# Optimization experiments

Hardware: AMD Instinct MI355X
Metric: run time of the kernel (lower is better)

Reference implementation:

```python
import jax, jax.numpy as jnp
import numpy as np
import math

N = 50000      # nodes per view
E = 800000     # edges per view (avg degree 16)
V = 2          # number of views / adjacencies
F_IN = 500     # input feature dim per view
C = 128        # nhidden
L = 4          # nlayers
NCLASS = 16
K_ATT = 5      # ECA kernel: t=int((log2(128)+1)/2)=4 -> even -> k=5
ALPHA = 0.1
LAMDA = 0.5


def setup_inputs() -> dict:
    key = jax.random.key(0)
    ks = jax.random.split(key, 12)
    glorot = lambda k, shp: jax.random.uniform(k, shp, jnp.float32, -1.0, 1.0) * np.sqrt(6.0 / (shp[-1] + shp[-2]))
    return {
        'x': jax.random.normal(ks[0], (V, N, F_IN), jnp.float32),
        'rows': jax.random.randint(ks[1], (V, E), 0, N, jnp.int32),
        'cols': jax.random.randint(ks[2], (V, E), 0, N, jnp.int32),
        # normalized-adjacency-like values, ~1/deg so spmm output stays O(1)
        'vals': jax.random.uniform(ks[3], (V, E), jnp.float32) / 16.0,
        'fc_w': glorot(ks[4], (V, C, F_IN)),
        'fc_b': jnp.zeros((V, C), jnp.float32),
        'conv_w': glorot(ks[5], (L, C, C)),
        'att_conv_w': jax.random.normal(ks[6], (L, K_ATT), jnp.float32) * (1.0 / np.sqrt(K_ATT)),
        'att_fc_w': glorot(ks[7], (L, C, C)),
        'att_fc_b': jnp.zeros((L, C), jnp.float32),
        'att_mix_w': jnp.full((L,), -0.8, jnp.float32),
        'out_w': glorot(ks[8], (NCLASS, C)),
        'out_b': jnp.zeros((NCLASS,), jnp.float32),
    }


def _conv1d(x, w):
    # torch Conv1d(1,1,k,padding=k//2,bias=False) over channel axis; x:[N,C], w:[k]
    k = w.shape[0]
    pad = k // 2
    xp = jnp.pad(x, ((0, 0), (pad, pad)))
    c = x.shape[1]
    out = jnp.zeros_like(x)
    for j in range(k):  # k is small & static (5)
        out = out + w[j] * xp[:, j:j + c]
    return out


def _fc_attention(xv, cw, fw, fb, mw):
    # xv:[N,C]. AdaptiveAvgPool2d(1) on a [N,C,1,1] tensor is identity.
    x1 = _conv1d(xv, cw)                 # [N,C]
    x2 = xv @ fw.T + fb                  # 1x1 conv2d == linear, [N,C]
    # sum over dim=1 of the [N,C,C] outer products == (row-sum) * other vector
    s1 = jnp.sum(x1, axis=1, keepdims=True)
    s2 = jnp.sum(x2, axis=1, keepdims=True)
    out1 = jax.nn.sigmoid(s1 * x2)
    out2 = jax.nn.sigmoid(s2 * x1)
    m = jax.nn.sigmoid(mw)
    out = m * out1 + (1.0 - m) * out2
    out = jax.nn.sigmoid(_conv1d(out, cw))
    return xv * out, out


def _ortho_norm(W):
    wtw = W.T @ W + 1e-4 * jnp.eye(W.shape[1], dtype=W.dtype)
    Lc = jnp.linalg.cholesky(wtw)
    # W @ inv(Lc).T  ==  solve_triangular(Lc, W.T).T
    return jax.scipy.linalg.solve_triangular(Lc, W.T, lower=True).T


def _gcn_layer(h, r, c, v, h0, W, l):
    Wo = _ortho_norm(W)
    hi = jax.ops.segment_sum(v[:, None] * h[c], r, num_segments=h.shape[0])  # spmm
    support = (1.0 - ALPHA) * hi + ALPHA * h0
    theta = math.log(LAMDA / l + 1.0)
    out = theta * (support @ Wo) + (1.0 - theta) * support  # residual=False, variant=False
    return jnp.tanh(out)


def reference(x, rows, cols, vals, fc_w, fc_b, conv_w, att_conv_w, att_fc_w,
              att_fc_b, att_mix_w, out_w, out_b):
    weights_att = []
    outputs = []
    for k in range(V):
        h0 = jax.nn.relu(x[k] @ fc_w[k].T + fc_b[k])  # dropout is identity in eval
        h = h0
        for i in range(L):
            if k == 0:
                h, w_att = _fc_attention(h, att_conv_w[i], att_fc_w[i], att_fc_b[i], att_mix_w[i])
                weights_att.append(w_att)
                h = jax.nn.relu(_gcn_layer(h, rows[k], cols[k], vals[k], h0, conv_w[i], i + 1))
            else:
                h = jax.nn.relu(_gcn_layer(h, rows[k], cols[k], vals[k], h0, conv_w[i], i + 1))
                h = h * weights_att[i]
        outputs.append(h)
    logits = [o @ out_w.T + out_b for o in outputs]
    total = logits[0]
    for lg in logits[1:]:
        total = total + lg
    lsm = [jax.nn.log_softmax(lg, axis=1) for lg in logits]
    mean_out = jnp.mean(jnp.stack(lsm), axis=0)
    return (jax.nn.log_softmax(total, axis=1), mean_out, lsm[0], lsm[1])
```

## Files before the change

### kernel.cpp

```cpp
#include <hip/hip_runtime.h>
#include <hip/hip_bf16.h>
#include <math.h>

static const int N_NODES = 50000;
static const int N_EDGES = 800000;
static const int F_IN    = 500;
static const int C_DIM   = 128;

using bf16x8 = __attribute__((ext_vector_type(8))) short;
using f32x4  = __attribute__((ext_vector_type(4))) float;

__device__ __forceinline__ float sigmoidf_(float x) { return 1.f / (1.f + __expf(-x)); }

__device__ __forceinline__ unsigned short f2bf(float f) {
    __hip_bfloat16 h = __float2bfloat16(f);
    unsigned short u;
    __builtin_memcpy(&u, &h, 2);
    return u;
}

__global__ __launch_bounds__(256) void wtw_kernel(const float* __restrict__ conv_w,
                                                  float* __restrict__ Am_g)
{
    __shared__ float Wi[128][16];
    __shared__ float Wj[128][16];
    const int bid = blockIdx.x;
    const int li  = bid >> 6;
    const int t6  = bid & 63;
    const int ti  = (t6 >> 3) << 4;
    const int tj  = (t6 & 7) << 4;
    const int tid = threadIdx.x;
    const float* W = conv_w + (size_t)li * 16384;
    for (int idx = tid; idx < 2048; idx += 256) {
        int k = idx >> 4, c = idx & 15;
        Wi[k][c] = W[k * 128 + ti + c];
        Wj[k][c] = W[k * 128 + tj + c];
    }
    __syncthreads();
    const int i = tid >> 4, j = tid & 15;
    float acc = 0.f;
    for (int k = 0; k < 128; ++k) acc = fmaf(Wi[k][i], Wj[k][j], acc);
    if (ti + i == tj + j) acc += 1e-4f;
    Am_g[(size_t)li * 16384 + (ti + i) * 128 + tj + j] = acc;
}

__global__ __launch_bounds__(512) void chol_solve_kernel(const float* __restrict__ Am_g,
                                                         const float* __restrict__ conv_w,
                                                         unsigned short* __restrict__ woT)
{
    __shared__ float Am[128][129];
    __shared__ float Wm[128][129];
    const int li  = blockIdx.x;
    const int tid = threadIdx.x;
    const float* Ag = Am_g  + (size_t)li * 16384;
    const float* Wg = conv_w + (size_t)li * 16384;
    for (int idx = tid; idx < 16384; idx += 512) {
        Am[idx >> 7][idx & 127] = Ag[idx];
        Wm[idx >> 7][idx & 127] = Wg[idx];
    }
    __syncthreads();

    for (int k = 0; k < 127; ++k) {
        float rk = 1.f / Am[k][k];
        const int R = 127 - k;
        for (int idx = tid; idx < (R << 7); idx += 512) {
            int i2 = k + 1 + (idx >> 7);
            int j  = idx & 127;
            if (j > k && j <= i2)
                Am[i2][j] = fmaf(-Am[i2][k] * rk, Am[j][k], Am[i2][j]);
        }
        __syncthreads();
    }

    for (int p = 0; p < 4; ++p) {
        const int kbase = p * 32;
        if (p > 0) {
            const int kk = tid & 31, k = kbase + kk;
            const int jb = (tid >> 5) * 8;
            float a0=0,a1=0,a2=0,a3=0,a4=0,a5=0,a6=0,a7=0;
            for (int m = 0; m < kbase; ++m) {
                float am = Am[k][m];
                a0 = fmaf(am, Wm[jb+0][m], a0); a1 = fmaf(am, Wm[jb+1][m], a1);
                a2 = fmaf(am, Wm[jb+2][m], a2); a3 = fmaf(am, Wm[jb+3][m], a3);
                a4 = fmaf(am, Wm[jb+4][m], a4); a5 = fmaf(am, Wm[jb+5][m], a5);
                a6 = fmaf(am, Wm[jb+6][m], a6); a7 = fmaf(am, Wm[jb+7][m], a7);
            }
            Wm[jb+0][k] -= a0; Wm[jb+1][k] -= a1; Wm[jb+2][k] -= a2; Wm[jb+3][k] -= a3;
            Wm[jb+4][k] -= a4; Wm[jb+5][k] -= a5; Wm[jb+6][k] -= a6; Wm[jb+7][k] -= a7;
        }
        __syncthreads();
        if (tid < 128) {
            const int j = tid;
            for (int kk = 0; kk < 32; ++kk) {
                int k = kbase + kk;
                float num = Wm[j][k];
                for (int m = kbase; m < k; ++m) num = fmaf(-Am[k][m], Wm[j][m], num);
                Wm[j][k] = num / Am[k][k];
            }
        }
        __syncthreads();
    }

    unsigned short* o = woT + (size_t)li * 16384;
    for (int idx = tid; idx < 16384; idx += 512) {
        int a = idx >> 7, b = idx & 127;
        o[idx] = f2bf(Wm[b][a] * sqrtf(Am[a][a]));
    }
}

__global__ __launch_bounds__(256) void conv_attw_kernel(const float* __restrict__ w,
                                                        unsigned short* __restrict__ o)
{
    int idx = blockIdx.x * 256 + threadIdx.x;
    if (idx < 65536) o[idx] = f2bf(w[idx]);
}

__global__ __launch_bounds__(256) void conv_fcw_kernel(const float* __restrict__ w,
                                                       unsigned short* __restrict__ o)
{
    int idx = blockIdx.x * 256 + threadIdx.x;
    if (idx >= 131072) return;
    int row = idx >> 9, k = idx & 511;
    o[idx] = (k < 500) ? f2bf(w[row * 500 + k]) : (unsigned short)0;
}


__global__ __launch_bounds__(256) void fc_relu_mfma_kernel(const float* __restrict__ x,
                                                           const unsigned short* __restrict__ wbf,
                                                           const float* __restrict__ b,
                                                           float* __restrict__ h0,
                                                           float* __restrict__ h1,
                                                           int nrows)
{
    __shared__ unsigned short Asm[64 * 136];
    __shared__ unsigned short Bsm[128 * 136];
    const int tid  = threadIdx.x;
    const int n0   = blockIdx.x * 64;
    const int lane = tid & 63;
    const int wv   = tid >> 6;
    const int lrow = lane & 15;
    const int kgrp = lane >> 4;

    f32x4 acc[8];
#pragma unroll
    for (int t = 0; t < 8; ++t) acc[t] = (f32x4){0.f, 0.f, 0.f, 0.f};

    for (int kc = 0; kc < 512; kc += 128) {
        for (int cid = tid; cid < 128 * 16; cid += 256) {
            int r = cid >> 4, c8 = cid & 15;
            *reinterpret_cast<bf16x8*>(&Bsm[r * 136 + c8 * 8]) =
                *reinterpret_cast<const bf16x8*>(&wbf[r * 512 + kc + c8 * 8]);
        }
        for (int cid = tid; cid < 64 * 16; cid += 256) {
            int r = cid >> 4, c8 = cid & 15;
            int n = n0 + r;
            int kg = kc + c8 * 8;
            union { unsigned short u[8]; bf16x8 v; } t;
            if (n < nrows && kg + 8 <= 500) {
                const float* src = &x[(size_t)n * 500 + kg];
                float4 v0 = *reinterpret_cast<const float4*>(src);
                float4 v1 = *reinterpret_cast<const float4*>(src + 4);
                t.u[0]=f2bf(v0.x); t.u[1]=f2bf(v0.y); t.u[2]=f2bf(v0.z); t.u[3]=f2bf(v0.w);
                t.u[4]=f2bf(v1.x); t.u[5]=f2bf(v1.y); t.u[6]=f2bf(v1.z); t.u[7]=f2bf(v1.w);
            } else if (n < nrows) {
#pragma unroll
                for (int e = 0; e < 8; ++e)
                    t.u[e] = (kg + e < 500) ? f2bf(x[(size_t)n * 500 + kg + e]) : (unsigned short)0;
            } else {
#pragma unroll
                for (int e = 0; e < 8; ++e) t.u[e] = 0;
            }
            *reinterpret_cast<bf16x8*>(&Asm[r * 136 + c8 * 8]) = t.v;
        }
        __syncthreads();
#pragma unroll
        for (int kt = 0; kt < 4; ++kt) {
            int koff = kt * 32 + kgrp * 8;
            bf16x8 av = *reinterpret_cast<const bf16x8*>(&Asm[(wv * 16 + lrow) * 136 + koff]);
#pragma unroll
            for (int t = 0; t < 8; ++t) {
                bf16x8 bv = *reinterpret_cast<const bf16x8*>(&Bsm[(t * 16 + lrow) * 136 + koff]);
                acc[t] = __builtin_amdgcn_mfma_f32_16x16x32_bf16(av, bv, acc[t], 0, 0, 0);
            }
        }
        __syncthreads();
    }
#pragma unroll
    for (int t = 0; t < 8; ++t) {
        int j = t * 16 + lrow;
        float bj = b[j];
#pragma unroll
        for (int r = 0; r < 4; ++r) {
            int n = n0 + wv * 16 + kgrp * 4 + r;
            if (n < nrows) {
                float v = fmaxf(acc[t][r] + bj, 0.f);
                h0[(size_t)n * 128 + j] = v;
                h1[(size_t)n * 128 + j] = v;
            }
        }
    }
}

template <int MODE>
__global__ __launch_bounds__(256) void gemm128_mfma_kernel(const float* __restrict__ A0,
                                                           const float* __restrict__ A1,
                                                           const unsigned short* __restrict__ Bw,
                                                           const float* __restrict__ bias,
                                                           const float* __restrict__ watt,
                                                           float* __restrict__ outp,
                                                           float c0, float c1, float theta,
                                                           int nrows)
{
    __shared__ unsigned short Asm[64 * 136];
    __shared__ unsigned short Bsm[128 * 136];
    const int tid  = threadIdx.x;
    const int n0   = blockIdx.x * 64;
    const int lane = tid & 63;
    const int wv   = tid >> 6;
    const int lrow = lane & 15;
    const int kgrp = lane >> 4;

    for (int cid = tid; cid < 128 * 16; cid += 256) {
        int r = cid >> 4, c8 = cid & 15;
        *reinterpret_cast<bf16x8*>(&Bsm[r * 136 + c8 * 8]) =
            *reinterpret_cast<const bf16x8*>(&Bw[r * 128 + c8 * 8]);
    }
    for (int cid = tid; cid < 64 * 16; cid += 256) {
        int r = cid >> 4, c8 = cid & 15;
        int n = n0 + r;
        union { unsigned short u[8]; bf16x8 v; } t;
        if (n < nrows) {
            const float* s0 = &A0[(size_t)n * 128 + c8 * 8];
            float4 a0 = *reinterpret_cast<const float4*>(s0);
            float4 a1 = *reinterpret_cast<const float4*>(s0 + 4);
            if (MODE == 1) {
                const float* s1 = &A1[(size_t)n * 128 + c8 * 8];
                float4 b0 = *reinterpret_cast<const float4*>(s1);
                float4 b1 = *reinterpret_cast<const float4*>(s1 + 4);
                a0.x = c0 * a0.x + c1 * b0.x; a0.y = c0 * a0.y + c1 * b0.y;
                a0.z = c0 * a0.z + c1 * b0.z; a0.w = c0 * a0.w + c1 * b0.w;
                a1.x = c0 * a1.x + c1 * b1.x; a1.y = c0 * a1.y + c1 * b1.y;
                a1.z = c0 * a1.z + c1 * b1.z; a1.w = c0 * a1.w + c1 * b1.w;
            }
            t.u[0]=f2bf(a0.x); t.u[1]=f2bf(a0.y); t.u[2]=f2bf(a0.z); t.u[3]=f2bf(a0.w);
            t.u[4]=f2bf(a1.x); t.u[5]=f2bf(a1.y); t.u[6]=f2bf(a1.z); t.u[7]=f2bf(a1.w);
        } else {
#pragma unroll
            for (int e = 0; e < 8; ++e) t.u[e] = 0;
        }
        *reinterpret_cast<bf16x8*>(&Asm[r * 136 + c8 * 8]) = t.v;
    }
    __syncthreads();

    f32x4 acc[8];
#pragma unroll
    for (int t = 0; t < 8; ++t) acc[t] = (f32x4){0.f, 0.f, 0.f, 0.f};
#pragma unroll
    for (int kt = 0; kt < 4; ++kt) {
        int koff = kt * 32 + kgrp * 8;
        bf16x8 av = *reinterpret_cast<const bf16x8*>(&Asm[(wv * 16 + lrow) * 136 + koff]);
#pragma unroll
        for (int t = 0; t < 8; ++t) {
            bf16x8 bv = *reinterpret_cast<const bf16x8*>(&Bsm[(t * 16 + lrow) * 136 + koff]);
            acc[t] = __builtin_amdgcn_mfma_f32_16x16x32_bf16(av, bv, acc[t], 0, 0, 0);
        }
    }

#pragma unroll
    for (int t = 0; t < 8; ++t) {
        int j = t * 16 + lrow;
#pragma unroll
        for (int r = 0; r < 4; ++r) {
            int n = n0 + wv * 16 + kgrp * 4 + r;
            if (n >= nrows) continue;
            float v = acc[t][r];
            if (MODE == 0) {
                v += bias[j];
            } else {
                float s = c0 * A0[(size_t)n * 128 + j] + c1 * A1[(size_t)n * 128 + j];
                v = theta * v + (1.f - theta) * s;
                v = tanhf(v);
                v = fmaxf(v, 0.f);
                if (watt) v *= watt[(size_t)n * 128 + j];
            }
            outp[(size_t)n * 128 + j] = v;
        }
    }
}

__global__ __launch_bounds__(256) void att_kernel(float* __restrict__ h,
                                                  const float* __restrict__ x2g,
                                                  const float* __restrict__ cw,
                                                  const float* __restrict__ mwp,
                                                  float* __restrict__ watt,
                                                  int nrows)
{
    __shared__ float hrow[2][132];
    __shared__ float orow[2][132];
    __shared__ float red[2][2][2];
    const int tid = threadIdx.x;
    const int c   = tid & 127;
    const int rl  = tid >> 7;
    const int n   = blockIdx.x * 2 + rl;
    const bool valid = n < nrows;
    float hv = 0.f, x2v = 0.f;
    if (valid) { hv = h[(size_t)n * 128 + c]; x2v = x2g[(size_t)n * 128 + c]; }
    hrow[rl][c + 2] = hv;
    if (c < 2) { hrow[rl][c] = 0.f; hrow[rl][c + 130] = 0.f; }
    const float w0 = cw[0], w1 = cw[1], w2 = cw[2], w3 = cw[3], w4 = cw[4];
    __syncthreads();
    float x1 = w0 * hrow[rl][c] + w1 * hrow[rl][c + 1] + w2 * hrow[rl][c + 2]
             + w3 * hrow[rl][c + 3] + w4 * hrow[rl][c + 4];
    float p1 = x1, p2 = x2v;
#pragma unroll
    for (int off = 32; off; off >>= 1) { p1 += __shfl_xor(p1, off); p2 += __shfl_xor(p2, off); }
    int wir = (tid >> 6) & 1;
    if ((tid & 63) == 0) { red[rl][0][wir] = p1; red[rl][1][wir] = p2; }
    __syncthreads();
    float s1 = red[rl][0][0] + red[rl][0][1];
    float s2 = red[rl][1][0] + red[rl][1][1];
    float m  = sigmoidf_(mwp[0]);
    float o  = m * sigmoidf_(s1 * x2v) + (1.f - m) * sigmoidf_(s2 * x1);
    orow[rl][c + 2] = o;
    if (c < 2) { orow[rl][c] = 0.f; orow[rl][c + 130] = 0.f; }
    __syncthreads();
    float wv = w0 * orow[rl][c] + w1 * orow[rl][c + 1] + w2 * orow[rl][c + 2]
             + w3 * orow[rl][c + 3] + w4 * orow[rl][c + 4];
    wv = sigmoidf_(wv);
    if (valid) {
        watt[(size_t)n * 128 + c] = wv;
        h[(size_t)n * 128 + c]    = hv * wv;
    }
}

__global__ __launch_bounds__(256) void hist_kernel(const int* __restrict__ rows,
                                                   int* __restrict__ rcnt)
{
    int gid = blockIdx.x * 256 + threadIdx.x;
    if (gid >= 2 * N_EDGES) return;
    int vsel = (gid >= N_EDGES) ? 1 : 0;
    atomicAdd(&rcnt[vsel * N_NODES + rows[gid]], 1);
}

__global__ __launch_bounds__(1024) void scan_kernel(int* __restrict__ rcnt)
{
    __shared__ int s[2][1024];
    int* c = rcnt + blockIdx.x * N_NODES;
    const int tid = threadIdx.x;
    int running = 0;
    for (int base = 0; base < N_NODES; base += 1024) {
        int idx = base + tid;
        int val = (idx < N_NODES) ? c[idx] : 0;
        int buf = 0;
        s[0][tid] = val;
        __syncthreads();
#pragma unroll
        for (int off = 1; off < 1024; off <<= 1) {
            int t = s[buf][tid];
            if (tid >= off) t += s[buf][tid - off];
            s[buf ^ 1][tid] = t;
            buf ^= 1;
            __syncthreads();
        }
        int excl = s[buf][tid] - val;
        if (idx < N_NODES) c[idx] = running + excl;
        running += s[buf][1023];
        __syncthreads();
    }
}

__global__ __launch_bounds__(256) void scatter_kernel(const int* __restrict__ rows,
                                                      const int* __restrict__ cols,
                                                      const float* __restrict__ vals,
                                                      int* __restrict__ rcnt,
                                                      int* __restrict__ scol,
                                                      float* __restrict__ sval)
{
    int gid = blockIdx.x * 256 + threadIdx.x;
    if (gid >= 2 * N_EDGES) return;
    int vsel = (gid >= N_EDGES) ? 1 : 0;
    int pos = atomicAdd(&rcnt[vsel * N_NODES + rows[gid]], 1);
    scol[vsel * N_EDGES + pos] = cols[gid];
    sval[vsel * N_EDGES + pos] = vals[gid];
}

__global__ __launch_bounds__(256) void spmm_csr_kernel(const int* __restrict__ rend,
                                                       const int* __restrict__ scol,
                                                       const float* __restrict__ sval,
                                                       const float* __restrict__ h,
                                                       float* __restrict__ hi)
{
    const int tid  = threadIdx.x;
    const int row  = blockIdx.x * 8 + (tid >> 5);
    if (row >= N_NODES) return;
    const int lane = tid & 31;
    const int c0   = lane * 4;
    const int beg  = (row == 0) ? 0 : rend[row - 1];
    const int end  = rend[row];
    float4 acc = {0.f, 0.f, 0.f, 0.f};
    for (int e = beg; e < end; ++e) {
        int   c = scol[e];
        float v = sval[e];
        const float4 hv = *reinterpret_cast<const float4*>(&h[(size_t)c * 128 + c0]);
        acc.x += v * hv.x; acc.y += v * hv.y; acc.z += v * hv.z; acc.w += v * hv.w;
    }
    *reinterpret_cast<float4*>(&hi[(size_t)row * 128 + c0]) = acc;
}

__global__ __launch_bounds__(256) void out_kernel(const float* __restrict__ hA,
                                                  const float* __restrict__ hB,
                                                  const float* __restrict__ ow,
                                                  const float* __restrict__ ob,
                                                  float* __restrict__ outp,
                                                  int nrows)
{
    const int tid  = threadIdx.x;
    const int lane = tid & 63;
    const int wid  = tid >> 6;
    const int n    = blockIdx.x * 4 + wid;
    if (n >= nrows) return;
    const int j   = lane & 15;
    const int seg = lane >> 4;
    const float* a  = &hA[(size_t)n * 128 + seg * 32];
    const float* bx = &hB[(size_t)n * 128 + seg * 32];
    const float* wj = &ow[j * 128 + seg * 32];
    float d0 = 0.f, d1 = 0.f;
#pragma unroll
    for (int k = 0; k < 32; ++k) { float wv = wj[k]; d0 += a[k] * wv; d1 += bx[k] * wv; }
    d0 += __shfl_xor(d0, 16); d0 += __shfl_xor(d0, 32);
    d1 += __shfl_xor(d1, 16); d1 += __shfl_xor(d1, 32);
    float bias = ob[j];
    float l0 = d0 + bias, l1 = d1 + bias, lt = l0 + l1;

    float mt = lt, m0 = l0, m1 = l1;
#pragma unroll
    for (int off = 8; off; off >>= 1) {
        mt = fmaxf(mt, __shfl_xor(mt, off));
        m0 = fmaxf(m0, __shfl_xor(m0, off));
        m1 = fmaxf(m1, __shfl_xor(m1, off));
    }
    float et = __expf(lt - mt), e0 = __expf(l0 - m0), e1 = __expf(l1 - m1);
    float st = et, s0 = e0, s1 = e1;
#pragma unroll
    for (int off = 8; off; off >>= 1) {
        st += __shfl_xor(st, off);
        s0 += __shfl_xor(s0, off);
        s1 += __shfl_xor(s1, off);
    }
    float ot  = lt - mt - __logf(st);
    float o0  = l0 - m0 - __logf(s0);
    float o1  = l1 - m1 - __logf(s1);
    if (lane < 16) {
        size_t base = (size_t)n * 16 + j;
        outp[0 * 800000 + base] = ot;
        outp[1 * 800000 + base] = 0.5f * (o0 + o1);
        outp[2 * 800000 + base] = o0;
        outp[3 * 800000 + base] = o1;
    }
}

extern "C" void kernel_launch(void* const* d_in, const int* in_sizes, int n_in,
                              void* d_out, int out_size, void* d_ws, size_t ws_size,
                              hipStream_t stream)
{
    const float* x          = (const float*)d_in[0];
    const int*   rows       = (const int*)d_in[1];
    const int*   cols       = (const int*)d_in[2];
    const float* vals       = (const float*)d_in[3];
    const float* fc_w       = (const float*)d_in[4];
    const float* fc_b       = (const float*)d_in[5];
    const float* conv_w     = (const float*)d_in[6];
    const float* att_conv_w = (const float*)d_in[7];
    const float* att_fc_w   = (const float*)d_in[8];
    const float* att_fc_b   = (const float*)d_in[9];
    const float* att_mix_w  = (const float*)d_in[10];
    const float* out_w      = (const float*)d_in[11];
    const float* out_b      = (const float*)d_in[12];
    float* outp = (float*)d_out;

    const size_t SB = (size_t)N_NODES * 128;
    float* ws     = (float*)d_ws;
    float* B_h0a  = ws + 0 * SB;
    float* B_h0b  = ws + 1 * SB;
    float* B_hA   = ws + 2 * SB;
    float* B_hB   = ws + 3 * SB;
    float* B_hi   = ws + 4 * SB;
    float* B_watt = ws + 5 * SB;
    float* extra  = ws + 6 * SB;
    unsigned short* WoT_bf  = (unsigned short*)extra;
    unsigned short* attw_bf = (unsigned short*)(extra + 32768);
    unsigned short* fcw_bf  = (unsigned short*)(extra + 65536);
    float*          Am_g    = extra + 131072;
    float* csr0   = extra + 196608;
    int*   rcnt   = (int*)csr0;
    int*   scol   = (int*)(csr0 + 2 * N_NODES);
    float* sval   = csr0 + 2 * N_NODES + 2 * N_EDGES;

    static const float thetas[4] = {0.40546511f, 0.22314355f, 0.15415068f, 0.11778304f};

    hipMemsetAsync(rcnt, 0, 2 * N_NODES * sizeof(int), stream);
    hist_kernel<<<6250, 256, 0, stream>>>(rows, rcnt);
    scan_kernel<<<2, 1024, 0, stream>>>(rcnt);
    scatter_kernel<<<6250, 256, 0, stream>>>(rows, cols, vals, rcnt, scol, sval);

    wtw_kernel<<<256, 256, 0, stream>>>(conv_w, Am_g);
    conv_attw_kernel<<<256, 256, 0, stream>>>(att_fc_w, attw_bf);
    conv_fcw_kernel<<<512, 256, 0, stream>>>(fc_w, fcw_bf);
    chol_solve_kernel<<<4, 512, 0, stream>>>(Am_g, conv_w, WoT_bf);

    fc_relu_mfma_kernel<<<782, 256, 0, stream>>>(x, fcw_bf, fc_b, B_h0a, B_hA, N_NODES);
    fc_relu_mfma_kernel<<<782, 256, 0, stream>>>(x + (size_t)N_NODES * F_IN,
                                                 fcw_bf + 128 * 512, fc_b + 128,
                                                 B_h0b, B_hB, N_NODES);

    for (int i = 0; i < 4; ++i) {
        gemm128_mfma_kernel<0><<<782, 256, 0, stream>>>(B_hA, nullptr,
                                                        attw_bf + (size_t)i * 16384,
                                                        att_fc_b + i * 128, nullptr,
                                                        B_hi, 1.f, 0.f, 0.f, N_NODES);
        att_kernel<<<25000, 256, 0, stream>>>(B_hA, B_hi, att_conv_w + i * 5,
                                              att_mix_w + i, B_watt, N_NODES);
        spmm_csr_kernel<<<6250, 256, 0, stream>>>(rcnt, scol, sval, B_hA, B_hi);
        gemm128_mfma_kernel<1><<<782, 256, 0, stream>>>(B_hi, B_h0a, WoT_bf + (size_t)i * 16384,
                                                        nullptr, nullptr, B_hA,
                                                        0.9f, 0.1f, thetas[i], N_NODES);
        spmm_csr_kernel<<<6250, 256, 0, stream>>>(rcnt + N_NODES, scol + N_EDGES,
                                                  sval + N_EDGES, B_hB, B_hi);
        gemm128_mfma_kernel<1><<<782, 256, 0, stream>>>(B_hi, B_h0b, WoT_bf + (size_t)i * 16384,
                                                        nullptr, B_watt, B_hB,
                                                        0.9f, 0.1f, thetas[i], N_NODES);
    }

    out_kernel<<<12500, 256, 0, stream>>>(B_hA, B_hB, out_w, out_b, outp, N_NODES);
}
```

Baseline: 1.981 ms.

## Store activations as bf16, fuse h0 mixing into SpMM, block the Cholesky factorization

The SpMM now gathers bf16 neighbor rows instead of fp32, which halves gather bandwidth. It also folds the 0.9/0.1 initial-residual mix with h0 into its epilogue and writes a bf16 support tensor. The GEMM then loads that tensor directly, with no second fp32 operand read or re-conversion. The attention weights and h0 are kept as bf16, and the Cholesky is restructured into 32-wide panels with a 4x4 register-tiled trailing update to cut synchronizations. The cost is reduced precision: the residual term and the SpMM inputs are now rounded to bf16.

New measurement: 1.660 ms. 1.19x faster.

```diff
diff --git a/kernel.cpp b/kernel.cpp
--- a/kernel.cpp
+++ b/kernel.cpp
@@ -17,6 +17,12 @@
     unsigned short u;
     __builtin_memcpy(&u, &h, 2);
     return u;
+}
+__device__ __forceinline__ float bflo(unsigned int w) {
+    unsigned int u = w << 16; float f; __builtin_memcpy(&f, &u, 4); return f;
+}
+__device__ __forceinline__ float bfhi(unsigned int w) {
+    unsigned int u = w & 0xffff0000u; float f; __builtin_memcpy(&f, &u, 4); return f;
 }
 
 __global__ __launch_bounds__(256) void wtw_kernel(const float* __restrict__ conv_w,
@@ -50,6 +56,7 @@
 {
     __shared__ float Am[128][129];
     __shared__ float Wm[128][129];
+    __shared__ float rkv[32];
     const int li  = blockIdx.x;
     const int tid = threadIdx.x;
     const float* Ag = Am_g  + (size_t)li * 16384;
@@ -60,16 +67,64 @@
     }
     __syncthreads();
 
-    for (int k = 0; k < 127; ++k) {
-        float rk = 1.f / Am[k][k];
-        const int R = 127 - k;
-        for (int idx = tid; idx < (R << 7); idx += 512) {
-            int i2 = k + 1 + (idx >> 7);
-            int j  = idx & 127;
-            if (j > k && j <= i2)
-                Am[i2][j] = fmaf(-Am[i2][k] * rk, Am[j][k], Am[i2][j]);
-        }
+    for (int p = 0; p < 4; ++p) {
+        const int kb = p * 32;
+        for (int kk = 0; kk < 31; ++kk) {
+            const int k  = kb + kk;
+            const float rk = 1.f / Am[k][k];
+            const int R  = 31 - kk;
+            for (int idx = tid; idx < R * 32; idx += 512) {
+                int i = k + 1 + (idx >> 5);
+                int j = kb + (idx & 31);
+                if (j > k && j <= i)
+                    Am[i][j] = fmaf(-Am[i][k] * rk, Am[j][k], Am[i][j]);
+            }
+            __syncthreads();
+        }
+        if (tid < 32) rkv[tid] = 1.f / Am[kb + tid][kb + tid];
         __syncthreads();
+
+        if (p < 3) {
+            const int tb = kb + 32;
+            const int TR = 128 - tb;
+            if (tid < TR) {
+                const int i = tb + tid;
+                for (int kk = 0; kk < 31; ++kk) {
+                    const int k = kb + kk;
+                    const float f = Am[i][k] * rkv[kk];
+                    for (int j = k + 1; j < kb + 32; ++j)
+                        Am[i][j] = fmaf(-f, Am[j][k], Am[i][j]);
+                }
+            }
+            __syncthreads();
+            const int nt = TR >> 2;
+            for (int t = tid; t < nt * nt; t += 512) {
+                const int ti = t / nt, tj = t - ti * nt;
+                if (ti < tj) continue;
+                const int i0 = tb + ti * 4, j0 = tb + tj * 4;
+                float acc[4][4] = {};
+                for (int kk = 0; kk < 32; ++kk) {
+                    const int k = kb + kk;
+                    const float rk = rkv[kk];
+                    float ai[4], aj[4];
+#pragma unroll
+                    for (int r = 0; r < 4; ++r) ai[r] = Am[i0 + r][k];
+#pragma unroll
+                    for (int c = 0; c < 4; ++c) aj[c] = Am[j0 + c][k] * rk;
+#pragma unroll
+                    for (int r = 0; r < 4; ++r)
+#pragma unroll
+                        for (int c = 0; c < 4; ++c)
+                            acc[r][c] = fmaf(ai[r], aj[c], acc[r][c]);
+                }
+#pragma unroll
+                for (int r = 0; r < 4; ++r)
+#pragma unroll
+                    for (int c = 0; c < 4; ++c)
+                        Am[i0 + r][j0 + c] -= acc[r][c];
+            }
+            __syncthreads();
+        }
     }
 
     for (int p = 0; p < 4; ++p) {
@@ -128,8 +183,9 @@
 __global__ __launch_bounds__(256) void fc_relu_mfma_kernel(const float* __restrict__ x,
                                                            const unsigned short* __restrict__ wbf,
                                                            const float* __restrict__ b,
-                                                           float* __restrict__ h0,
+                                                           unsigned short* __restrict__ h0bf,
                                                            float* __restrict__ h1,
+                                                           unsigned short* __restrict__ h1bf,
                                                            int nrows)
 {
     __shared__ unsigned short Asm[64 * 136];
@@ -194,22 +250,24 @@
             int n = n0 + wv * 16 + kgrp * 4 + r;
             if (n < nrows) {
                 float v = fmaxf(acc[t][r] + bj, 0.f);
-                h0[(size_t)n * 128 + j] = v;
-                h1[(size_t)n * 128 + j] = v;
+                unsigned short vb = f2bf(v);
+                h0bf[(size_t)n * 128 + j] = vb;
+                h1[(size_t)n * 128 + j]  = v;
+                if (h1bf) h1bf[(size_t)n * 128 + j] = vb;
             }
         }
     }
 }
 
 template <int MODE>
-__global__ __launch_bounds__(256) void gemm128_mfma_kernel(const float* __restrict__ A0,
-                                                           const float* __restrict__ A1,
+__global__ __launch_bounds__(256) void gemm128_mfma_kernel(const float* __restrict__ A0f,
+                                                           const unsigned short* __restrict__ Abf,
                                                            const unsigned short* __restrict__ Bw,
                                                            const float* __restrict__ bias,
-                                                           const float* __restrict__ watt,
+                                                           const unsigned short* __restrict__ wattbf,
                                                            float* __restrict__ outp,
-                                                           float c0, float c1, float theta,
-                                                           int nrows)
+                                                           unsigned short* __restrict__ outbf,
+                                                           float theta, int nrows)
 {
     __shared__ unsigned short Asm[64 * 136];
     __shared__ unsigned short Bsm[128 * 136];
@@ -228,27 +286,25 @@
     for (int cid = tid; cid < 64 * 16; cid += 256) {
         int r = cid >> 4, c8 = cid & 15;
         int n = n0 + r;
-        union { unsigned short u[8]; bf16x8 v; } t;
-        if (n < nrows) {
-            const float* s0 = &A0[(size_t)n * 128 + c8 * 8];
-            float4 a0 = *reinterpret_cast<const float4*>(s0);
-            float4 a1 = *reinterpret_cast<const float4*>(s0 + 4);
-            if (MODE == 1) {
-                const float* s1 = &A1[(size_t)n * 128 + c8 * 8];
-                float4 b0 = *reinterpret_cast<const float4*>(s1);
-                float4 b1 = *reinterpret_cast<const float4*>(s1 + 4);
-                a0.x = c0 * a0.x + c1 * b0.x; a0.y = c0 * a0.y + c1 * b0.y;
-                a0.z = c0 * a0.z + c1 * b0.z; a0.w = c0 * a0.w + c1 * b0.w;
-                a1.x = c0 * a1.x + c1 * b1.x; a1.y = c0 * a1.y + c1 * b1.y;
-                a1.z = c0 * a1.z + c1 * b1.z; a1.w = c0 * a1.w + c1 * b1.w;
-            }
-            t.u[0]=f2bf(a0.x); t.u[1]=f2bf(a0.y); t.u[2]=f2bf(a0.z); t.u[3]=f2bf(a0.w);
-            t.u[4]=f2bf(a1.x); t.u[5]=f2bf(a1.y); t.u[6]=f2bf(a1.z); t.u[7]=f2bf(a1.w);
+        if (MODE == 1) {
+            bf16x8 v = {};
+            if (n < nrows)
+                v = *reinterpret_cast<const bf16x8*>(&Abf[(size_t)n * 128 + c8 * 8]);
+            *reinterpret_cast<bf16x8*>(&Asm[r * 136 + c8 * 8]) = v;
         } else {
-#pragma unroll
-            for (int e = 0; e < 8; ++e) t.u[e] = 0;
-        }
-        *reinterpret_cast<bf16x8*>(&Asm[r * 136 + c8 * 8]) = t.v;
+            union { unsigned short u[8]; bf16x8 v; } t;
+            if (n < nrows) {
+                const float* s0 = &A0f[(size_t)n * 128 + c8 * 8];
+                float4 a0 = *reinterpret_cast<const float4*>(s0);
+                float4 a1 = *reinterpret_cast<const float4*>(s0 + 4);
+                t.u[0]=f2bf(a0.x); t.u[1]=f2bf(a0.y); t.u[2]=f2bf(a0.z); t.u[3]=f2bf(a0.w);
+                t.u[4]=f2bf(a1.x); t.u[5]=f2bf(a1.y); t.u[6]=f2bf(a1.z); t.u[7]=f2bf(a1.w);
+            } else {
+#pragma unroll
+                for (int e = 0; e < 8; ++e) t.u[e] = 0;
+            }
+            *reinterpret_cast<bf16x8*>(&Asm[r * 136 + c8 * 8]) = t.v;
+        }
     }
     __syncthreads();
 
@@ -271,19 +327,21 @@
         int j = t * 16 + lrow;
 #pragma unroll
         for (int r = 0; r < 4; ++r) {
-            int n = n0 + wv * 16 + kgrp * 4 + r;
+            int rt = wv * 16 + kgrp * 4 + r;
+            int n  = n0 + rt;
             if (n >= nrows) continue;
             float v = acc[t][r];
             if (MODE == 0) {
                 v += bias[j];
             } else {
-                float s = c0 * A0[(size_t)n * 128 + j] + c1 * A1[(size_t)n * 128 + j];
+                float s = bflo((unsigned int)Asm[rt * 136 + j]);
                 v = theta * v + (1.f - theta) * s;
                 v = tanhf(v);
                 v = fmaxf(v, 0.f);
-                if (watt) v *= watt[(size_t)n * 128 + j];
+                if (wattbf) v *= bflo((unsigned int)wattbf[(size_t)n * 128 + j]);
             }
             outp[(size_t)n * 128 + j] = v;
+            if (MODE == 1 && outbf) outbf[(size_t)n * 128 + j] = f2bf(v);
         }
     }
 }
@@ -292,7 +350,8 @@
                                                   const float* __restrict__ x2g,
                                                   const float* __restrict__ cw,
                                                   const float* __restrict__ mwp,
-                                                  float* __restrict__ watt,
+                                                  unsigned short* __restrict__ wattbf,
+                                                  unsigned short* __restrict__ hbf,
                                                   int nrows)
 {
     __shared__ float hrow[2][132];
@@ -328,8 +387,10 @@
              + w3 * orow[rl][c + 3] + w4 * orow[rl][c + 4];
     wv = sigmoidf_(wv);
     if (valid) {
-        watt[(size_t)n * 128 + c] = wv;
-        h[(size_t)n * 128 + c]    = hv * wv;
+        float g = hv * wv;
+        wattbf[(size_t)n * 128 + c] = f2bf(wv);
+        h[(size_t)n * 128 + c]      = g;
+        hbf[(size_t)n * 128 + c]    = f2bf(g);
     }
 }
 
@@ -387,8 +448,9 @@
 __global__ __launch_bounds__(256) void spmm_csr_kernel(const int* __restrict__ rend,
                                                        const int* __restrict__ scol,
                                                        const float* __restrict__ sval,
-                                                       const float* __restrict__ h,
-                                                       float* __restrict__ hi)
+                                                       const unsigned short* __restrict__ hbf,
+                                                       const unsigned short* __restrict__ h0bf,
+                                                       unsigned short* __restrict__ suppbf)
 {
     const int tid  = threadIdx.x;
     const int row  = blockIdx.x * 8 + (tid >> 5);
@@ -397,14 +459,25 @@
     const int c0   = lane * 4;
     const int beg  = (row == 0) ? 0 : rend[row - 1];
     const int end  = rend[row];
-    float4 acc = {0.f, 0.f, 0.f, 0.f};
+    float a0 = 0.f, a1 = 0.f, a2 = 0.f, a3 = 0.f;
     for (int e = beg; e < end; ++e) {
         int   c = scol[e];
         float v = sval[e];
-        const float4 hv = *reinterpret_cast<const float4*>(&h[(size_t)c * 128 + c0]);
-        acc.x += v * hv.x; acc.y += v * hv.y; acc.z += v * hv.z; acc.w += v * hv.w;
-    }
-    *reinterpret_cast<float4*>(&hi[(size_t)row * 128 + c0]) = acc;
+        uint2 hv = *reinterpret_cast<const uint2*>(&hbf[(size_t)c * 128 + c0]);
+        a0 = fmaf(v, bflo(hv.x), a0);
+        a1 = fmaf(v, bfhi(hv.x), a1);
+        a2 = fmaf(v, bflo(hv.y), a2);
+        a3 = fmaf(v, bfhi(hv.y), a3);
+    }
+    uint2 h0v = *reinterpret_cast<const uint2*>(&h0bf[(size_t)row * 128 + c0]);
+    float s0 = 0.9f * a0 + 0.1f * bflo(h0v.x);
+    float s1 = 0.9f * a1 + 0.1f * bfhi(h0v.x);
+    float s2 = 0.9f * a2 + 0.1f * bflo(h0v.y);
+    float s3 = 0.9f * a3 + 0.1f * bfhi(h0v.y);
+    uint2 o;
+    o.x = (unsigned int)f2bf(s0) | ((unsigned int)f2bf(s1) << 16);
+    o.y = (unsigned int)f2bf(s2) | ((unsigned int)f2bf(s3) << 16);
+    *reinterpret_cast<uint2*>(&suppbf[(size_t)row * 128 + c0]) = o;
 }
 
 __global__ __launch_bounds__(256) void out_kernel(const float* __restrict__ hA,
@@ -478,23 +551,24 @@
     const float* out_b      = (const float*)d_in[12];
     float* outp = (float*)d_out;
 
-    const size_t SB = (size_t)N_NODES * 128;
-    float* ws     = (float*)d_ws;
-    float* B_h0a  = ws + 0 * SB;
-    float* B_h0b  = ws + 1 * SB;
-    float* B_hA   = ws + 2 * SB;
-    float* B_hB   = ws + 3 * SB;
-    float* B_hi   = ws + 4 * SB;
-    float* B_watt = ws + 5 * SB;
-    float* extra  = ws + 6 * SB;
-    unsigned short* WoT_bf  = (unsigned short*)extra;
-    unsigned short* attw_bf = (unsigned short*)(extra + 32768);
-    unsigned short* fcw_bf  = (unsigned short*)(extra + 65536);
-    float*          Am_g    = extra + 131072;
-    float* csr0   = extra + 196608;
-    int*   rcnt   = (int*)csr0;
-    int*   scol   = (int*)(csr0 + 2 * N_NODES);
-    float* sval   = csr0 + 2 * N_NODES + 2 * N_EDGES;
+    const size_t SBf = (size_t)N_NODES * 128;
+    char* base = (char*)d_ws;
+    float*          B_hA    = (float*)base;                         base += SBf * 4;
+    float*          B_hB    = (float*)base;                         base += SBf * 4;
+    float*          B_hi    = (float*)base;                         base += SBf * 4;
+    unsigned short* h0a_bf  = (unsigned short*)base;                base += SBf * 2;
+    unsigned short* h0b_bf  = (unsigned short*)base;                base += SBf * 2;
+    unsigned short* hA_bf   = (unsigned short*)base;                base += SBf * 2;
+    unsigned short* hB_bf   = (unsigned short*)base;                base += SBf * 2;
+    unsigned short* watt_bf = (unsigned short*)base;                base += SBf * 2;
+    unsigned short* supp_bf = (unsigned short*)base;                base += SBf * 2;
+    unsigned short* WoT_bf  = (unsigned short*)base;                base += 4 * 16384 * 2;
+    unsigned short* attw_bf = (unsigned short*)base;                base += 4 * 16384 * 2;
+    unsigned short* fcw_bf  = (unsigned short*)base;                base += 2 * 128 * 512 * 2;
+    float*          Am_g    = (float*)base;                         base += 4 * 16384 * 4;
+    int*            rcnt    = (int*)base;                           base += 2 * N_NODES * 4;
+    int*            scol    = (int*)base;                           base += 2 * N_EDGES * 4;
+    float*          sval    = (float*)base;
 
     static const float thetas[4] = {0.40546511f, 0.22314355f, 0.15415068f, 0.11778304f};
 
@@ -508,27 +582,30 @@
     conv_fcw_kernel<<<512, 256, 0, stream>>>(fc_w, fcw_bf);
     chol_solve_kernel<<<4, 512, 0, stream>>>(Am_g, conv_w, WoT_bf);
 
-    fc_relu_mfma_kernel<<<782, 256, 0, stream>>>(x, fcw_bf, fc_b, B_h0a, B_hA, N_NODES);
+    fc_relu_mfma_kernel<<<782, 256, 0, stream>>>(x, fcw_bf, fc_b,
+                                                 h0a_bf, B_hA, (unsigned short*)nullptr, N_NODES);
     fc_relu_mfma_kernel<<<782, 256, 0, stream>>>(x + (size_t)N_NODES * F_IN,
                                                  fcw_bf + 128 * 512, fc_b + 128,
-                                                 B_h0b, B_hB, N_NODES);
+                                                 h0b_bf, B_hB, hB_bf, N_NODES);
 
     for (int i = 0; i < 4; ++i) {
         gemm128_mfma_kernel<0><<<782, 256, 0, stream>>>(B_hA, nullptr,
                                                         attw_bf + (size_t)i * 16384,
                                                         att_fc_b + i * 128, nullptr,
-                                                        B_hi, 1.f, 0.f, 0.f, N_NODES);
+                                                        B_hi, nullptr, 0.f, N_NODES);
         att_kernel<<<25000, 256, 0, stream>>>(B_hA, B_hi, att_conv_w + i * 5,
-                                              att_mix_w + i, B_watt, N_NODES);
-        spmm_csr_kernel<<<6250, 256, 0, stream>>>(rcnt, scol, sval, B_hA, B_hi);
-        gemm128_mfma_kernel<1><<<782, 256, 0, stream>>>(B_hi, B_h0a, WoT_bf + (size_t)i * 16384,
-                                                        nullptr, nullptr, B_hA,
-                                                        0.9f, 0.1f, thetas[i], N_NODES);
+                                              att_mix_w + i, watt_bf, hA_bf, N_NODES);
+        spmm_csr_kernel<<<6250, 256, 0, stream>>>(rcnt, scol, sval, hA_bf, h0a_bf, supp_bf);
+        gemm128_mfma_kernel<1><<<782, 256, 0, stream>>>(nullptr, supp_bf,
+                                                        WoT_bf + (size_t)i * 16384,
+                                                        nullptr, nullptr,
+                                                        B_hA, nullptr, thetas[i], N_NODES);
         spmm_csr_kernel<<<6250, 256, 0, stream>>>(rcnt + N_NODES, scol + N_EDGES,
-                                                  sval + N_EDGES, B_hB, B_hi);
-        gemm128_mfma_kernel<1><<<782, 256, 0, stream>>>(B_hi, B_h0b, WoT_bf + (size_t)i * 16384,
-                                                        nullptr, B_watt, B_hB,
-                                                        0.9f, 0.1f, thetas[i], N_NODES);
+                                                  sval + N_EDGES, hB_bf, h0b_bf, supp_bf);
+        gemm128_mfma_kernel<1><<<782, 256, 0, stream>>>(nullptr, supp_bf,
+                                                        WoT_bf + (size_t)i * 16384,
+                                                        nullptr, watt_bf,
+                                                        B_hB, hB_bf, thetas[i], N_NODES);
     }
 
     out_kernel<<<12500, 256, 0, stream>>>(B_hA, B_hB, out_w, out_b, outp, N_NODES);
```
